# Kernel optimization log

Measured on AMD Instinct MI355X. Metric: run time of the kernel, lower is better.

Reference implementation:

```python
import jax, jax.numpy as jnp
import numpy as np

N_BATCH, N_ATOMS = 64, 2048
NODES = [384, 128, 96, 2]
N_ELEMENTS = 4


def _glorot(key, fan_in, fan_out, n_experts):
    scale = (2.0 / (fan_in + fan_out)) ** 0.5
    return (jax.random.normal(key, (n_experts, fan_in, fan_out), dtype=jnp.float32) * scale)


def setup_inputs() -> dict:
    key = jax.random.key(0)
    ks = jax.random.split(key, 6)
    elements = jax.random.randint(ks[0], (N_BATCH, N_ATOMS), 0, N_ELEMENTS)
    features = jax.random.normal(ks[1], (N_BATCH, N_ATOMS, NODES[0]), dtype=jnp.float32)
    # Per-element expert MLP params, stacked over the element axis [E, in, out].
    W1 = _glorot(ks[2], NODES[0], NODES[1], N_ELEMENTS)
    b1 = jnp.zeros((N_ELEMENTS, NODES[1]), dtype=jnp.float32)
    W2 = _glorot(ks[3], NODES[1], NODES[2], N_ELEMENTS)
    b2 = jnp.zeros((N_ELEMENTS, NODES[2]), dtype=jnp.float32)
    W3 = _glorot(ks[4], NODES[2], NODES[3], N_ELEMENTS)
    b3 = jnp.zeros((N_ELEMENTS, NODES[3]), dtype=jnp.float32)
    return {"elements": elements, "features": features,
            "W1": W1, "b1": b1, "W2": W2, "b2": b2, "W3": W3, "b3": b3}


def reference(elements, features, W1, b1, W2, b2, W3, b3):
    n, m, f = features.shape
    x = features.reshape(n * m, f)           # [T, f] flattened tokens
    el = elements.reshape(-1)                # [T]
    n_experts = W1.shape[0]
    out_dim = W3.shape[-1]
    y = jnp.zeros((n * m, out_dim), dtype=features.dtype)
    # Fixed small loop over element-specific experts (dispatch/combine via mask).
    for e in range(n_experts):
        h = jax.nn.celu(x @ W1[e] + b1[e])
        h = jax.nn.celu(h @ W2[e] + b2[e])
        o = h @ W3[e] + b3[e]
        y = jnp.where((el == e)[:, None], o, y)
    return elements, y.reshape(n, m, out_dim)
```

## Files before the change

kernel.cpp:

```cpp
#include <hip/hip_runtime.h>
#include <math.h>

#define F_IN    384
#define N1      128
#define N2      96
#define N3      2
#define NEXP    4
#define BM      64

typedef __attribute__((ext_vector_type(8))) short           bf16x8;
typedef __attribute__((ext_vector_type(4))) float           f32x4;
typedef __attribute__((ext_vector_type(4))) unsigned short  us4;
typedef __attribute__((ext_vector_type(8))) unsigned short  us8;

__device__ __forceinline__ unsigned short f2bf(float f) {
  unsigned int u = __float_as_uint(f);
  return (unsigned short)((u + 0x7FFFu + ((u >> 16) & 1u)) >> 16);
}


__global__ __launch_bounds__(256) void hist_kernel(
    const int* __restrict__ el, float* __restrict__ out_el,
    int* __restrict__ counts, int T) {
  int t = blockIdx.x * blockDim.x + threadIdx.x;
  if (t >= T) return;
  int e = el[t];
  out_el[t] = (float)e;
#pragma unroll
  for (int v = 0; v < NEXP; ++v) {
    unsigned long long m = __ballot(e == v);
    if (e == v) {
      int lane = threadIdx.x & 63;
      int leader = __ffsll(m) - 1;
      if (lane == leader) atomicAdd(&counts[v], __popcll(m));
    }
  }
}

__global__ void scan_kernel(int* __restrict__ ws) {
  if (threadIdx.x == 0) {
    int o = 0;
#pragma unroll
    for (int e = 0; e < NEXP; ++e) {
      ws[4 + e] = o;
      ws[8 + e] = o;
      o += ws[e];
    }
  }
}

__global__ __launch_bounds__(256) void scatter_kernel(
    const int* __restrict__ el, int* __restrict__ cursors,
    int* __restrict__ list, int T) {
  int t = blockIdx.x * blockDim.x + threadIdx.x;
  if (t >= T) return;
  int e = el[t];
  int lane = threadIdx.x & 63;
  unsigned long long lt = (lane == 0) ? 0ull : ((~0ull) >> (64 - lane));
#pragma unroll
  for (int v = 0; v < NEXP; ++v) {
    unsigned long long m = __ballot(e == v);
    if (e == v) {
      int leader = __ffsll(m) - 1;
      int prefix = __popcll(m & lt);
      int base = 0;
      if (lane == leader) base = atomicAdd(&cursors[v], __popcll(m));
      base = __shfl(base, leader, 64);
      list[base + prefix] = t;
    }
  }
}

__global__ __launch_bounds__(256) void prep_weights(
    const float* __restrict__ W1, const float* __restrict__ W2,
    unsigned short* __restrict__ Wt1, unsigned short* __restrict__ Wt2) {
  int i = blockIdx.x * 256 + threadIdx.x;
  const int n1 = NEXP * N1 * F_IN;
  if (i < n1) {
    int e = i / (N1 * F_IN), r = i % (N1 * F_IN);
    int n = r / F_IN, k = r % F_IN;
    Wt1[i] = f2bf(W1[(e * F_IN + k) * N1 + n]);
  } else {
    int j = i - n1;
    if (j < NEXP * N2 * N1) {
      int e = j / (N2 * N1), r = j % (N2 * N1);
      int n = r / N1, k = r % N1;
      Wt2[j] = f2bf(W2[(e * N1 + k) * N2 + n]);
    }
  }
}

__global__ __launch_bounds__(256) void moe_mlp_mfma(
    const float* __restrict__ X,
    const float* __restrict__ b1, const float* __restrict__ b2,
    const float* __restrict__ W3, const float* __restrict__ b3,
    const int* __restrict__ ws_i,
    const unsigned short* __restrict__ Wt1,
    const unsigned short* __restrict__ Wt2,
    float* __restrict__ Y, int T) {
  const int e = blockIdx.y;
  const int cnt = ws_i[e];
  const int m0 = blockIdx.x * BM;
  if (m0 >= cnt) return;
  const int* list = ws_i + 16 + ws_i[4 + e];

  __shared__ __align__(16) unsigned short arena[13184];
  __shared__ int toks[BM];
  unsigned short* XsU  = arena;
  unsigned short* Ws1U = arena + 2560;
  unsigned short* HU   = arena;
  unsigned short* Ws2U = arena + 8704;
  float* H2f = (float*)arena;
  float* W3s = (float*)(arena + 12800);

  const int tid  = threadIdx.x;
  const int lane = tid & 63;
  const int w    = tid >> 6;
  const int ln15 = lane & 15;
  const int g    = lane >> 4;

  if (tid < BM) {
    int gi = m0 + tid;
    toks[tid] = (gi < cnt) ? list[gi] : -1;
  }
  __syncthreads();

  const int wr = w >> 1, wc = w & 1;
  f32x4 acc[2][4];
#pragma unroll
  for (int i = 0; i < 2; ++i)
#pragma unroll
    for (int j = 0; j < 4; ++j) acc[i][j] = (f32x4){0.f, 0.f, 0.f, 0.f};

  const unsigned short* Wt1e = Wt1 + (size_t)e * (N1 * F_IN);
  for (int ks = 0; ks < F_IN / 32; ++ks) {
    const int k0 = ks * 32;
#pragma unroll
    for (int p = 0; p < 2; ++p) {
      int q = p * 256 + tid;
      int m = q >> 3, kq = (q & 7) * 4;
      int tok = toks[m];
      float4 v = make_float4(0.f, 0.f, 0.f, 0.f);
      if (tok >= 0) v = *(const float4*)&X[(size_t)tok * F_IN + k0 + kq];
      us4 b4; b4.x = f2bf(v.x); b4.y = f2bf(v.y); b4.z = f2bf(v.z); b4.w = f2bf(v.w);
      *(us4*)&XsU[m * 40 + kq] = b4;
    }
#pragma unroll
    for (int p = 0; p < 2; ++p) {
      int q = p * 256 + tid;
      int n = q >> 2, h = q & 3;
      *(us8*)&Ws1U[n * 40 + h * 8] = *(const us8*)&Wt1e[n * F_IN + k0 + h * 8];
    }
    __syncthreads();

    bf16x8 af[2], bf[4];
#pragma unroll
    for (int rt = 0; rt < 2; ++rt)
      af[rt] = *(const bf16x8*)&XsU[(wr * 32 + rt * 16 + ln15) * 40 + g * 8];
#pragma unroll
    for (int ct = 0; ct < 4; ++ct)
      bf[ct] = *(const bf16x8*)&Ws1U[(wc * 64 + ct * 16 + ln15) * 40 + g * 8];
#pragma unroll
    for (int rt = 0; rt < 2; ++rt)
#pragma unroll
      for (int ct = 0; ct < 4; ++ct)
        acc[rt][ct] = __builtin_amdgcn_mfma_f32_16x16x32_bf16(
            af[rt], bf[ct], acc[rt][ct], 0, 0, 0);
    __syncthreads();
  }

#pragma unroll
  for (int rt = 0; rt < 2; ++rt)
#pragma unroll
    for (int ct = 0; ct < 4; ++ct) {
      int c = wc * 64 + ct * 16 + ln15;
      float bias = b1[e * N1 + c];
#pragma unroll
      for (int r = 0; r < 4; ++r) {
        float v = acc[rt][ct][r] + bias;
        v = v > 0.f ? v : expm1f(v);
        HU[(wr * 32 + rt * 16 + g * 4 + r) * 136 + c] = f2bf(v);
      }
    }
  __syncthreads();

  f32x4 acc2[6];
#pragma unroll
  for (int j = 0; j < 6; ++j) acc2[j] = (f32x4){0.f, 0.f, 0.f, 0.f};

  const unsigned short* Wt2e = Wt2 + (size_t)e * (N2 * N1);
  for (int ks = 0; ks < N1 / 32; ++ks) {
    const int k0 = ks * 32;
#pragma unroll
    for (int p = 0; p < 2; ++p) {
      int q = p * 256 + tid;
      if (q < 384) {
        int n = q >> 2, h = q & 3;
        *(us8*)&Ws2U[n * 40 + h * 8] = *(const us8*)&Wt2e[n * N1 + k0 + h * 8];
      }
    }
    __syncthreads();

    bf16x8 a = *(const bf16x8*)&HU[(w * 16 + ln15) * 136 + k0 + g * 8];
#pragma unroll
    for (int ct = 0; ct < 6; ++ct) {
      bf16x8 b = *(const bf16x8*)&Ws2U[(ct * 16 + ln15) * 40 + g * 8];
      acc2[ct] = __builtin_amdgcn_mfma_f32_16x16x32_bf16(a, b, acc2[ct], 0, 0, 0);
    }
    __syncthreads();
  }

#pragma unroll
  for (int ct = 0; ct < 6; ++ct) {
    int c = ct * 16 + ln15;
    float bias = b2[e * N2 + c];
#pragma unroll
    for (int r = 0; r < 4; ++r) {
      float v = acc2[ct][r] + bias;
      v = v > 0.f ? v : expm1f(v);
      H2f[(w * 16 + g * 4 + r) * 100 + c] = v;
    }
  }
  if (tid < N2 * N3) W3s[tid] = W3[e * N2 * N3 + tid];
  __syncthreads();

  if (tid < BM * N3) {
    const int m = tid >> 1;
    const int c = tid & 1;
    float s = b3[e * N3 + c];
#pragma unroll
    for (int k4 = 0; k4 < N2; k4 += 4) {
      const float4 h = *(const float4*)&H2f[m * 100 + k4];
      s = fmaf(h.x, W3s[(k4 + 0) * N3 + c], s);
      s = fmaf(h.y, W3s[(k4 + 1) * N3 + c], s);
      s = fmaf(h.z, W3s[(k4 + 2) * N3 + c], s);
      s = fmaf(h.w, W3s[(k4 + 3) * N3 + c], s);
    }
    const int tok = toks[m];
    if (tok >= 0) Y[(size_t)tok * N3 + c] = s;
  }
}

extern "C" void kernel_launch(void* const* d_in, const int* in_sizes, int n_in,
                              void* d_out, int out_size, void* d_ws, size_t ws_size,
                              hipStream_t stream) {
  const int*   elements = (const int*)d_in[0];
  const float* X  = (const float*)d_in[1];
  const float* W1 = (const float*)d_in[2];
  const float* b1 = (const float*)d_in[3];
  const float* W2 = (const float*)d_in[4];
  const float* b2 = (const float*)d_in[5];
  const float* W3 = (const float*)d_in[6];
  const float* b3 = (const float*)d_in[7];
  const int T = in_sizes[0];

  float* out    = (float*)d_out;
  float* out_el = out;
  float* Y      = out + T;

  int* ws_i    = (int*)d_ws;
  int* counts  = ws_i;
  int* cursors = ws_i + 8;
  int* list    = ws_i + 16;

  size_t wt1_off = ((size_t)64 + 4 * (size_t)T + 63) & ~(size_t)63;
  unsigned short* Wt1 = (unsigned short*)((char*)d_ws + wt1_off);
  unsigned short* Wt2 = Wt1 + NEXP * N1 * F_IN;

  hipMemsetAsync(ws_i, 0, 16 * sizeof(int), stream);
  int nb = (T + 255) / 256;
  hist_kernel<<<nb, 256, 0, stream>>>(elements, out_el, counts, T);
  scan_kernel<<<1, 64, 0, stream>>>(ws_i);
  scatter_kernel<<<nb, 256, 0, stream>>>(elements, cursors, list, T);
  prep_weights<<<(NEXP * N1 * F_IN + NEXP * N2 * N1 + 255) / 256, 256, 0, stream>>>(
      W1, W2, Wt1, Wt2);
  dim3 grid((T + BM - 1) / BM, NEXP);
  moe_mlp_mfma<<<grid, 256, 0, stream>>>(X, b1, b2, W3, b3, ws_i, Wt1, Wt2, Y, T);
}
```

Before: 532.7 us.

## Load MFMA operands directly from global memory, dropping LDS staging in both GEMMs

Layer 1 and layer 2 now read the activation and weight fragments for each MFMA straight from global memory into registers, with no LDS staging tiles. The per-k-step block barriers go away and the K loops are fully unrolled. Each wave now owns 16 rows across all 128 output columns rather than a 32x64 tile, so weight fragments are fetched redundantly by every wave and rely on L1/L2 for reuse. Padded rows now read token 0 instead of zeros, and those results are discarded at the store.

```diff
diff --git a/kernel.cpp b/kernel.cpp
--- a/kernel.cpp
+++ b/kernel.cpp
@@ -10,7 +10,6 @@
 
 typedef __attribute__((ext_vector_type(8))) short           bf16x8;
 typedef __attribute__((ext_vector_type(4))) float           f32x4;
-typedef __attribute__((ext_vector_type(4))) unsigned short  us4;
 typedef __attribute__((ext_vector_type(8))) unsigned short  us8;
 
 __device__ __forceinline__ unsigned short f2bf(float f) {
@@ -106,10 +105,7 @@
 
   __shared__ __align__(16) unsigned short arena[13184];
   __shared__ int toks[BM];
-  unsigned short* XsU  = arena;
-  unsigned short* Ws1U = arena + 2560;
-  unsigned short* HU   = arena;
-  unsigned short* Ws2U = arena + 8704;
+  unsigned short* HU  = arena;
   float* H2f = (float*)arena;
   float* W3s = (float*)(arena + 12800);
 
@@ -125,95 +121,69 @@
   }
   __syncthreads();
 
-  const int wr = w >> 1, wc = w & 1;
-  f32x4 acc[2][4];
-#pragma unroll
-  for (int i = 0; i < 2; ++i)
-#pragma unroll
-    for (int j = 0; j < 4; ++j) acc[i][j] = (f32x4){0.f, 0.f, 0.f, 0.f};
-
-  const unsigned short* Wt1e = Wt1 + (size_t)e * (N1 * F_IN);
+  const int myrow = w * 16 + ln15;
+  const int mytok = toks[myrow];
+  const int saferow = mytok < 0 ? 0 : mytok;
+  const float* xrow = X + (size_t)saferow * F_IN + g * 8;
+
+  f32x4 acc[8];
+#pragma unroll
+  for (int j = 0; j < 8; ++j) acc[j] = (f32x4){0.f, 0.f, 0.f, 0.f};
+
+  const unsigned short* Wt1e =
+      Wt1 + (size_t)e * (N1 * F_IN) + (size_t)ln15 * F_IN + g * 8;
+#pragma unroll
   for (int ks = 0; ks < F_IN / 32; ++ks) {
     const int k0 = ks * 32;
-#pragma unroll
-    for (int p = 0; p < 2; ++p) {
-      int q = p * 256 + tid;
-      int m = q >> 3, kq = (q & 7) * 4;
-      int tok = toks[m];
-      float4 v = make_float4(0.f, 0.f, 0.f, 0.f);
-      if (tok >= 0) v = *(const float4*)&X[(size_t)tok * F_IN + k0 + kq];
-      us4 b4; b4.x = f2bf(v.x); b4.y = f2bf(v.y); b4.z = f2bf(v.z); b4.w = f2bf(v.w);
-      *(us4*)&XsU[m * 40 + kq] = b4;
-    }
-#pragma unroll
-    for (int p = 0; p < 2; ++p) {
-      int q = p * 256 + tid;
-      int n = q >> 2, h = q & 3;
-      *(us8*)&Ws1U[n * 40 + h * 8] = *(const us8*)&Wt1e[n * F_IN + k0 + h * 8];
-    }
-    __syncthreads();
-
-    bf16x8 af[2], bf[4];
-#pragma unroll
-    for (int rt = 0; rt < 2; ++rt)
-      af[rt] = *(const bf16x8*)&XsU[(wr * 32 + rt * 16 + ln15) * 40 + g * 8];
-#pragma unroll
-    for (int ct = 0; ct < 4; ++ct)
-      bf[ct] = *(const bf16x8*)&Ws1U[(wc * 64 + ct * 16 + ln15) * 40 + g * 8];
-#pragma unroll
-    for (int rt = 0; rt < 2; ++rt)
-#pragma unroll
-      for (int ct = 0; ct < 4; ++ct)
-        acc[rt][ct] = __builtin_amdgcn_mfma_f32_16x16x32_bf16(
-            af[rt], bf[ct], acc[rt][ct], 0, 0, 0);
-    __syncthreads();
-  }
-
-#pragma unroll
-  for (int rt = 0; rt < 2; ++rt)
-#pragma unroll
-    for (int ct = 0; ct < 4; ++ct) {
-      int c = wc * 64 + ct * 16 + ln15;
-      float bias = b1[e * N1 + c];
-#pragma unroll
-      for (int r = 0; r < 4; ++r) {
-        float v = acc[rt][ct][r] + bias;
-        v = v > 0.f ? v : expm1f(v);
-        HU[(wr * 32 + rt * 16 + g * 4 + r) * 136 + c] = f2bf(v);
-      }
-    }
+    float4 lo = *(const float4*)&xrow[k0];
+    float4 hi = *(const float4*)&xrow[k0 + 4];
+    us8 a8;
+    a8[0] = f2bf(lo.x); a8[1] = f2bf(lo.y); a8[2] = f2bf(lo.z); a8[3] = f2bf(lo.w);
+    a8[4] = f2bf(hi.x); a8[5] = f2bf(hi.y); a8[6] = f2bf(hi.z); a8[7] = f2bf(hi.w);
+    bf16x8 af = *(bf16x8*)&a8;
+#pragma unroll
+    for (int ct = 0; ct < 8; ++ct) {
+      bf16x8 bf = *(const bf16x8*)&Wt1e[ct * 16 * F_IN + k0];
+      acc[ct] = __builtin_amdgcn_mfma_f32_16x16x32_bf16(af, bf, acc[ct], 0, 0, 0);
+    }
+  }
+
+#pragma unroll
+  for (int ct = 0; ct < 8; ++ct) {
+    const int c = ct * 16 + ln15;
+    const float bias = b1[e * N1 + c];
+#pragma unroll
+    for (int r = 0; r < 4; ++r) {
+      float v = acc[ct][r] + bias;
+      v = v > 0.f ? v : expm1f(v);
+      HU[(w * 16 + g * 4 + r) * 136 + c] = f2bf(v);
+    }
+  }
   __syncthreads();
 
   f32x4 acc2[6];
 #pragma unroll
   for (int j = 0; j < 6; ++j) acc2[j] = (f32x4){0.f, 0.f, 0.f, 0.f};
 
-  const unsigned short* Wt2e = Wt2 + (size_t)e * (N2 * N1);
+  const unsigned short* Wt2e =
+      Wt2 + (size_t)e * (N2 * N1) + (size_t)ln15 * N1 + g * 8;
+  const unsigned short* Hrow = &HU[myrow * 136 + g * 8];
+#pragma unroll
   for (int ks = 0; ks < N1 / 32; ++ks) {
     const int k0 = ks * 32;
-#pragma unroll
-    for (int p = 0; p < 2; ++p) {
-      int q = p * 256 + tid;
-      if (q < 384) {
-        int n = q >> 2, h = q & 3;
-        *(us8*)&Ws2U[n * 40 + h * 8] = *(const us8*)&Wt2e[n * N1 + k0 + h * 8];
-      }
-    }
-    __syncthreads();
-
-    bf16x8 a = *(const bf16x8*)&HU[(w * 16 + ln15) * 136 + k0 + g * 8];
+    bf16x8 a2 = *(const bf16x8*)&Hrow[k0];
 #pragma unroll
     for (int ct = 0; ct < 6; ++ct) {
-      bf16x8 b = *(const bf16x8*)&Ws2U[(ct * 16 + ln15) * 40 + g * 8];
-      acc2[ct] = __builtin_amdgcn_mfma_f32_16x16x32_bf16(a, b, acc2[ct], 0, 0, 0);
-    }
-    __syncthreads();
-  }
+      bf16x8 b2f = *(const bf16x8*)&Wt2e[ct * 16 * N1 + k0];
+      acc2[ct] = __builtin_amdgcn_mfma_f32_16x16x32_bf16(a2, b2f, acc2[ct], 0, 0, 0);
+    }
+  }
+  __syncthreads();
 
 #pragma unroll
   for (int ct = 0; ct < 6; ++ct) {
-    int c = ct * 16 + ln15;
-    float bias = b2[e * N2 + c];
+    const int c = ct * 16 + ln15;
+    const float bias = b2[e * N2 + c];
 #pragma unroll
     for (int r = 0; r < 4; ++r) {
       float v = acc2[ct][r] + bias;
```

Result: slower. 591.4 us (+11.0%).
